# Kernel optimization log

Hardware: AMD Instinct MI355X
Metric: run time of the kernel (lower is better)

## Reference

```python
import jax, jax.numpy as jnp
import numpy as np

N, E, B = 100000, 1600000, 1024
F, H, C = 9, 4, 32
CH, L = 30, 20

def _leaky(x, slope):
    return jnp.where(x >= 0, x, slope * x)

def _add_self_loops(edge_index, n):
    ar = jnp.arange(n, dtype=edge_index.dtype)
    return jnp.concatenate([edge_index, jnp.stack([ar, ar])], axis=1)

def _gat_conv(x, edge_index, W, att_src, att_dst, bias):
    # PyG GATConv, concat heads, eval mode (no attn dropout), self loops
    n = x.shape[0]
    ei = _add_self_loops(edge_index, n)
    src, dst = ei[0], ei[1]
    h = (x @ W).reshape(n, H, C)                      # [N,H,C]
    a_s = jnp.sum(h * att_src, axis=-1)               # [N,H]
    a_d = jnp.sum(h * att_dst, axis=-1)               # [N,H]
    e = _leaky(a_s[src] + a_d[dst], 0.2)              # [Etot,H]
    m = jax.ops.segment_max(e, dst, num_segments=n)
    ex = jnp.exp(e - m[dst])
    s = jax.ops.segment_sum(ex, dst, num_segments=n)
    alpha = ex / (s[dst] + 1e-16)                     # softmax per dst node/head
    msg = h[src] * alpha[:, :, None]                  # [Etot,H,C]
    out = jax.ops.segment_sum(msg, dst, num_segments=n)
    return out.reshape(n, H * C) + bias

def _gcn_conv(x, edge_index, W, bias):
    # PyG GCNConv: self loops + symmetric normalization
    n = x.shape[0]
    ei = _add_self_loops(edge_index, n)
    src, dst = ei[0], ei[1]
    deg = jax.ops.segment_sum(jnp.ones(ei.shape[1], x.dtype), dst, num_segments=n)
    dinv = jnp.where(deg > 0, jax.lax.rsqrt(deg), 0.0)
    norm = dinv[src] * dinv[dst]                      # [Etot]
    h = x @ W
    out = jax.ops.segment_sum(h[src] * norm[:, None], dst, num_segments=n)
    return out + bias

def _global_mean_pool(x, batch, b):
    s = jax.ops.segment_sum(x, batch, num_segments=b)
    cnt = jax.ops.segment_sum(jnp.ones(x.shape[0], x.dtype), batch, num_segments=b)
    return s / jnp.maximum(cnt, 1.0)[:, None]

def _conv1d(x, w, b):
    # x: [B,Cin,L], w: [Cout,Cin,K], VALID conv
    y = jax.lax.conv_general_dilated(x, w, (1,), 'VALID',
                                     dimension_numbers=('NCH', 'OIH', 'NCH'))
    return y + b[None, :, None]

def _bn_eval(x, g, be, m, v):
    return (x - m[None, :, None]) * jax.lax.rsqrt(v[None, :, None] + 1e-5) * g[None, :, None] + be[None, :, None]

def _forward(x, seq_data, W_gat, att_src, att_dst, b_gat, W2, b2, W3, b3,
             conv1_w, conv1_b, conv2_w, conv2_b,
             bn1_g, bn1_b, bn1_m, bn1_v, bn2_g, bn2_b, bn2_m, bn2_v,
             fc1_W, fc1_b, fus_W, fus_b, cls1_W, cls1_b, cls3_W, cls3_b,
             edge_index, batch):
    slope = 0.01  # nn.LeakyReLU default
    # graph branch
    g = _leaky(_gat_conv(x, edge_index, W_gat, att_src, att_dst, b_gat), slope)
    g = _leaky(_gcn_conv(g, edge_index, W2, b2), slope)
    g = _leaky(_gcn_conv(g, edge_index, W3, b3), slope)
    g = _global_mean_pool(g, batch, B)                # [B,128]
    # sequence branch (eval mode: dropout = identity, BN uses running stats)
    s = _conv1d(seq_data, conv1_w, conv1_b)           # [B,64,18]
    s = _leaky(_bn_eval(s, bn1_g, bn1_b, bn1_m, bn1_v), slope)
    s = _conv1d(s, conv2_w, conv2_b)                  # [B,64,16]
    s = _leaky(_bn_eval(s, bn2_g, bn2_b, bn2_m, bn2_v), slope)
    s = s.reshape(s.shape[0], -1) @ fc1_W + fc1_b     # [B,64]
    # fusion + classifier
    comb = jnp.concatenate([g, s], axis=1)            # [B,192]
    comb = _leaky(comb @ fus_W + fus_b, slope)
    comb = _leaky(comb @ cls1_W + cls1_b, slope)
    return comb @ cls3_W + cls3_b                     # [B,1]

def setup_inputs():
    key = jax.random.key(0)
    ks = jax.random.split(key, 20)
    rn = lambda k, s, sc=0.1: jax.random.normal(k, s, dtype=jnp.float32) * sc
    return {
        'x': rn(ks[0], (N, F), 1.0),
        'edge_index': jax.random.randint(ks[1], (2, E), 0, N, dtype=jnp.int32),
        'batch': jnp.sort(jax.random.randint(ks[2], (N,), 0, B, dtype=jnp.int32)),
        'seq_data': rn(ks[3], (B, CH, L), 1.0),
        'W_gat': rn(ks[4], (F, H * C)), 'att_src': rn(ks[5], (H, C)),
        'att_dst': rn(ks[6], (H, C)), 'b_gat': jnp.zeros(H * C, jnp.float32),
        'W2': rn(ks[7], (H * C, 64)), 'b2': jnp.zeros(64, jnp.float32),
        'W3': rn(ks[8], (64, 128)), 'b3': jnp.zeros(128, jnp.float32),
        'conv1_w': rn(ks[9], (64, CH, 3)), 'conv1_b': jnp.zeros(64, jnp.float32),
        'conv2_w': rn(ks[10], (64, 64, 3)), 'conv2_b': jnp.zeros(64, jnp.float32),
        'bn1_g': jnp.ones(64, jnp.float32), 'bn1_b': jnp.zeros(64, jnp.float32),
        'bn1_m': jnp.zeros(64, jnp.float32), 'bn1_v': jnp.ones(64, jnp.float32),
        'bn2_g': jnp.ones(64, jnp.float32), 'bn2_b': jnp.zeros(64, jnp.float32),
        'bn2_m': jnp.zeros(64, jnp.float32), 'bn2_v': jnp.ones(64, jnp.float32),
        'fc1_W': rn(ks[11], (16 * 64, 64)), 'fc1_b': jnp.zeros(64, jnp.float32),
        'fus_W': rn(ks[12], (192, 128)), 'fus_b': jnp.zeros(128, jnp.float32),
        'cls1_W': rn(ks[13], (128, 64)), 'cls1_b': jnp.zeros(64, jnp.float32),
        'cls3_W': rn(ks[14], (64, 1)), 'cls3_b': jnp.zeros(1, jnp.float32),
    }

def reference(x, edge_index, batch, seq_data, W_gat, att_src, att_dst, b_gat,
              W2, b2, W3, b3, conv1_w, conv1_b, conv2_w, conv2_b,
              bn1_g, bn1_b, bn1_m, bn1_v, bn2_g, bn2_b, bn2_m, bn2_v,
              fc1_W, fc1_b, fus_W, fus_b, cls1_W, cls1_b, cls3_W, cls3_b):
    return _forward(x, seq_data, W_gat, att_src, att_dst, b_gat, W2, b2, W3, b3,
                    conv1_w, conv1_b, conv2_w, conv2_b,
                    bn1_g, bn1_b, bn1_m, bn1_v, bn2_g, bn2_b, bn2_m, bn2_v,
                    fc1_W, fc1_b, fus_W, fus_b, cls1_W, cls1_b, cls3_W, cls3_b,
                    edge_index, batch)
```

## Files before the change

### kernel.cpp

```cpp
#include <hip/hip_runtime.h>

#define NND 100000
#define NED 1600000
#define NB  1024
#define FEAT 9
#define HC 128
#define NBUCK ((NND + 511) / 512)
#define BCAP 12288u
#define BINCHUNK 4096
#define BIN_NBLK ((NED + BINCHUNK - 1) / BINCHUNK)

typedef unsigned short u16;

__device__ __forceinline__ void atomAdd(float* p, float v) {
    __hip_atomic_fetch_add(p, v, __ATOMIC_RELAXED, __HIP_MEMORY_SCOPE_AGENT);
}
__device__ __forceinline__ unsigned atomAddU(unsigned* p, unsigned v) {
    return __hip_atomic_fetch_add(p, v, __ATOMIC_RELAXED, __HIP_MEMORY_SCOPE_AGENT);
}
__device__ __forceinline__ float leaky(float v, float s) { return v >= 0.f ? v : s * v; }
__device__ __forceinline__ float bf2f(u16 u) {
    union { unsigned i; float f; } x; x.i = ((unsigned)u) << 16; return x.f;
}
__device__ __forceinline__ u16 f2bf(float f) {
    union { float f; unsigned i; } x; x.f = f;
    return (u16)((x.i + 0x7fffu + ((x.i >> 16) & 1u)) >> 16);
}
__device__ __forceinline__ float bflo(unsigned u) {
    union { unsigned i; float f; } x; x.i = u << 16; return x.f;
}
__device__ __forceinline__ float bfhi(unsigned u) {
    union { unsigned i; float f; } x; x.i = u & 0xffff0000u; return x.f;
}

typedef __attribute__((ext_vector_type(8))) short bfrag;
typedef __attribute__((ext_vector_type(4))) float ffrag;

__global__ void k_matt(const float* __restrict__ Wg, const float* __restrict__ attS,
                       const float* __restrict__ attD, float* __restrict__ M) {
    int t = threadIdx.x;
    if (t >= 72) return;
    int d = t >= 36 ? 1 : 0;
    int q = t - 36 * d;
    int f = q >> 2, h = q & 3;
    const float* av = d ? attD : attS;
    float s = 0.f;
#pragma unroll
    for (int c = 0; c < 32; ++c) s += Wg[f * HC + h * 32 + c] * av[h * 32 + c];
    M[d * 36 + q] = s;
}

__global__ void k_w2t(const float* __restrict__ W2, const float* __restrict__ W3,
                      const float* __restrict__ Wg,
                      u16* __restrict__ w2t, u16* __restrict__ w3t,
                      u16* __restrict__ wgt, unsigned* __restrict__ bktCur) {
    int i = blockIdx.x * 256 + threadIdx.x;
    int n = i >> 7, k = i & 127;
    w2t[i] = f2bf(W2[k * 64 + n]);
    int n3 = i >> 6, k3 = i & 63;
    w3t[i] = f2bf(W3[k3 * 128 + n3]);
    int col = i >> 6, kk = i & 63;
    int f = kk - 9 * (col >> 5);
    wgt[i] = (f >= 0 && f < 9) ? f2bf(Wg[f * 128 + col]) : (u16)0;
    if (i < NBUCK) bktCur[i] = (unsigned)i * BCAP;
}

__global__ void k_att(const float* __restrict__ x, const float* __restrict__ M,
                      u16* __restrict__ rec, float* __restrict__ a_d) {
    __shared__ float Ms[36], Md[36];
    int t = threadIdx.x;
    if (t < 36) Ms[t] = M[t];
    else if (t < 72) Md[t - 36] = M[t];
    __syncthreads();
    int n = blockIdx.x * 256 + t;
    if (n >= NND) return;
    float xv[FEAT];
#pragma unroll
    for (int f = 0; f < FEAT; ++f) xv[f] = x[n * FEAT + f];
    float s0 = 0, s1 = 0, s2 = 0, s3 = 0, d0 = 0, d1 = 0, d2 = 0, d3 = 0;
#pragma unroll
    for (int f = 0; f < FEAT; ++f) {
        float xf = xv[f];
        s0 += xf * Ms[f * 4 + 0]; s1 += xf * Ms[f * 4 + 1];
        s2 += xf * Ms[f * 4 + 2]; s3 += xf * Ms[f * 4 + 3];
        d0 += xf * Md[f * 4 + 0]; d1 += xf * Md[f * 4 + 1];
        d2 += xf * Md[f * 4 + 2]; d3 += xf * Md[f * 4 + 3];
    }
    u16 v[16];
#pragma unroll
    for (int f = 0; f < FEAT; ++f) v[f] = f2bf(xv[f]);
    v[9] = 0; v[10] = 0; v[11] = 0;
    v[12] = f2bf(s0); v[13] = f2bf(s1); v[14] = f2bf(s2); v[15] = f2bf(s3);
    unsigned pk[8];
#pragma unroll
    for (int i = 0; i < 8; ++i) pk[i] = (unsigned)v[2 * i] | ((unsigned)v[2 * i + 1] << 16);
    uint4* rp = (uint4*)(rec + (size_t)n * 16);
    rp[0] = make_uint4(pk[0], pk[1], pk[2], pk[3]);
    rp[1] = make_uint4(pk[4], pk[5], pk[6], pk[7]);
    ((float4*)a_d)[n] = make_float4(d0, d1, d2, d3);
}

__global__ __launch_bounds__(256) void k_bin(const int* __restrict__ ei,
                                             unsigned* __restrict__ bktCursor,
                                             unsigned* __restrict__ staging) {
    __shared__ unsigned hist[NBUCK];
    __shared__ unsigned gbase[NBUCK];
    int t = threadIdx.x;
    if (t < NBUCK) hist[t] = 0;
    __syncthreads();
    int base = blockIdx.x * BINCHUNK;
    int lim = NED - base;
    int srcv[16], dstv[16];
#pragma unroll
    for (int k = 0; k < 16; ++k) {
        int i = t + k * 256;
        if (i < lim) {
            srcv[k] = ei[base + i];
            dstv[k] = ei[NED + base + i];
            atomicAdd(&hist[dstv[k] >> 9], 1u);
        } else dstv[k] = -1;
    }
    __syncthreads();
    if (t < NBUCK) {
        unsigned c = hist[t];
        gbase[t] = c ? atomAddU(&bktCursor[t], c) : 0u;
    }
    __syncthreads();
    if (t < NBUCK) hist[t] = 0;
    __syncthreads();
#pragma unroll
    for (int k = 0; k < 16; ++k) {
        if (dstv[k] >= 0) {
            int bk = dstv[k] >> 9;
            unsigned off = atomicAdd(&hist[bk], 1u);
            staging[gbase[bk] + off] = ((unsigned)(dstv[k] & 511) << 17) | (unsigned)srcv[k];
        }
    }
}

__global__ __launch_bounds__(512) void k_place(const unsigned* __restrict__ bktCur,
                                               const unsigned* __restrict__ staging,
                                               unsigned* __restrict__ csr,
                                               unsigned* __restrict__ rowptr,
                                               u16* __restrict__ degA,
                                               float* __restrict__ dinv) {
    __shared__ unsigned lh[512];
    __shared__ unsigned ls[512];
    int b = blockIdx.x, t = threadIdx.x;
    unsigned lo = (unsigned)b * BCAP;
    unsigned n = bktCur[b] - lo;
    lh[t] = 0;
    __syncthreads();
    for (unsigned i = t; i < n; i += 512) atomicAdd(&lh[staging[lo + i] >> 17], 1u);
    __syncthreads();
    unsigned v = lh[t];
    ls[t] = v;
    __syncthreads();
    for (int off = 1; off < 512; off <<= 1) {
        unsigned u = (t >= off) ? ls[t - off] : 0u;
        __syncthreads();
        ls[t] += u;
        __syncthreads();
    }
    unsigned excl = ls[t] - v;
    int node = b * 512 + t;
    if (node < NND) {
        rowptr[node] = lo + excl;
        degA[node] = (u16)v;
        dinv[node] = rsqrtf((float)v + 1.f);
    }
    __syncthreads();
    lh[t] = excl;
    __syncthreads();
    for (unsigned i = t; i < n; i += 512) {
        unsigned p = staging[lo + i];
        unsigned pos = atomicAdd(&lh[p >> 17], 1u);
        csr[lo + pos] = p & 0x1FFFFu;
    }
}

__global__ __launch_bounds__(256) void k_gat_g(const unsigned* __restrict__ rowptr,
                                               const u16* __restrict__ degA,
                                               const unsigned* __restrict__ csr,
                                               const u16* __restrict__ rec,
                                               const float* __restrict__ a_d,
                                               u16* __restrict__ zb) {
    int n = blockIdx.x * 4 + (threadIdx.x >> 6);
    int l = threadIdx.x & 63;
    int e = l >> 2;
    int h = l & 3;
    unsigned e0 = rowptr[n];
    int m = (int)degA[n] + 1;
    float adh = a_d[n * 4 + h];
    float acc0 = 0, acc1 = 0, acc2 = 0, acc3 = 0, acc4 = 0, acc5 = 0, acc6 = 0, acc7 = 0, acc8 = 0;
    float den = 0.f;
    const uint4* recp = (const uint4*)rec;
    for (int c = 0; c < m; c += 16) {
        int idx = c + e;
        bool act = idx < m;
        int src = n;
        if (act && idx > 0) src = (int)csr[e0 + idx - 1];
        uint4 lo = recp[(size_t)src * 2];
        uint4 hi = recp[(size_t)src * 2 + 1];
        unsigned pair = (h & 2) ? hi.w : hi.z;
        float asf = (h & 1) ? bfhi(pair) : bflo(pair);
        float w = __expf(leaky(asf + adh, 0.2f));
        if (!act) w = 0.f;
        den += w;
        acc0 += w * bflo(lo.x); acc1 += w * bfhi(lo.x);
        acc2 += w * bflo(lo.y); acc3 += w * bfhi(lo.y);
        acc4 += w * bflo(lo.z); acc5 += w * bfhi(lo.z);
        acc6 += w * bflo(lo.w); acc7 += w * bfhi(lo.w);
        acc8 += w * bflo(hi.x);
    }
#pragma unroll
    for (int mask = 4; mask <= 32; mask <<= 1) {
        den  += __shfl_xor(den,  mask, 64);
        acc0 += __shfl_xor(acc0, mask, 64);
        acc1 += __shfl_xor(acc1, mask, 64);
        acc2 += __shfl_xor(acc2, mask, 64);
        acc3 += __shfl_xor(acc3, mask, 64);
        acc4 += __shfl_xor(acc4, mask, 64);
        acc5 += __shfl_xor(acc5, mask, 64);
        acc6 += __shfl_xor(acc6, mask, 64);
        acc7 += __shfl_xor(acc7, mask, 64);
        acc8 += __shfl_xor(acc8, mask, 64);
    }
    if (l < 4) {
        float inv = 1.f / (den + 1e-16f);
        u16* zp = zb + (size_t)n * 36 + h * 9;
        zp[0] = f2bf(acc0 * inv); zp[1] = f2bf(acc1 * inv); zp[2] = f2bf(acc2 * inv);
        zp[3] = f2bf(acc3 * inv); zp[4] = f2bf(acc4 * inv); zp[5] = f2bf(acc5 * inv);
        zp[6] = f2bf(acc6 * inv); zp[7] = f2bf(acc7 * inv); zp[8] = f2bf(acc8 * inv);
    }
}

__global__ __launch_bounds__(256) void k_fused_h2(const u16* __restrict__ zb,
                                                  const u16* __restrict__ wgt,
                                                  const float* __restrict__ bgv,
                                                  const u16* __restrict__ w2t,
                                                  const float* __restrict__ dinv,
                                                  u16* __restrict__ h2) {
    __shared__ u16 zA[64 * 72];
    __shared__ u16 g1L[64 * 136];
    __shared__ float bgs[HC];
    int t = threadIdx.x;
    int n0 = blockIdx.x * 64;
    int nn = NND - n0; if (nn > 64) nn = 64;
    for (int i = t; i < 64 * 36; i += 256) ((unsigned*)zA)[i] = 0u;
    if (t < HC) bgs[t] = bgv[t];
    __syncthreads();
    const unsigned* zbG = (const unsigned*)zb;
    for (int i = t; i < nn * 18; i += 256) {
        int r = i / 18, c = i - r * 18;
        ((unsigned*)zA)[r * 36 + c] = zbG[(size_t)(n0 + r) * 18 + c];
    }
    __syncthreads();
    int l = t & 63, wv = t >> 6;
    int mr = l & 15, quad = l >> 4;
    union U { uint4 u; bfrag v; };
    {
        bfrag a[2];
#pragma unroll
        for (int ks = 0; ks < 2; ++ks) {
            U uu; uu.u = *(const uint4*)(zA + (wv * 16 + mr) * 72 + ks * 32 + quad * 8);
            a[ks] = uu.v;
        }
#pragma unroll
        for (int ct = 0; ct < 8; ++ct) {
            ffrag c = (ffrag){0.f, 0.f, 0.f, 0.f};
#pragma unroll
            for (int ks = 0; ks < 2; ++ks) {
                U ub; ub.u = *(const uint4*)(wgt + (ct * 16 + mr) * 64 + ks * 32 + quad * 8);
                c = __builtin_amdgcn_mfma_f32_16x16x32_bf16(a[ks], ub.v, c, 0, 0, 0);
            }
            int col = ct * 16 + mr;
            float bc = bgs[col];
#pragma unroll
            for (int r = 0; r < 4; ++r) {
                int row = wv * 16 + quad * 4 + r;
                g1L[row * 136 + col] = f2bf(leaky(c[r] + bc, 0.01f));
            }
        }
    }
    __syncthreads();
    {
        bfrag a[4];
#pragma unroll
        for (int ks = 0; ks < 4; ++ks) {
            U uu; uu.u = *(const uint4*)(g1L + (wv * 16 + mr) * 136 + ks * 32 + quad * 8);
            a[ks] = uu.v;
        }
        ffrag acc[4];
#pragma unroll
        for (int ct = 0; ct < 4; ++ct) acc[ct] = (ffrag){0.f, 0.f, 0.f, 0.f};
#pragma unroll
        for (int ct = 0; ct < 4; ++ct) {
#pragma unroll
            for (int ks = 0; ks < 4; ++ks) {
                U ub; ub.u = *(const uint4*)(w2t + (ct * 16 + mr) * 128 + ks * 32 + quad * 8);
                acc[ct] = __builtin_amdgcn_mfma_f32_16x16x32_bf16(a[ks], ub.v, acc[ct], 0, 0, 0);
            }
        }
        int rbase = n0 + wv * 16 + quad * 4;
        if (rbase < NND) {
            float4 d4 = *(const float4*)(dinv + rbase);
            const float dv[4] = {d4.x, d4.y, d4.z, d4.w};
#pragma unroll
            for (int ct = 0; ct < 4; ++ct)
#pragma unroll
                for (int r = 0; r < 4; ++r)
                    h2[(size_t)(rbase + r) * 64 + ct * 16 + mr] = f2bf(dv[r] * acc[ct][r]);
        }
    }
}

template <int OUTMODE>
__global__ void k_gcn_g(const unsigned* __restrict__ rowptr, const u16* __restrict__ degA,
                        const unsigned* __restrict__ csr,
                        const float* __restrict__ dinv, const u16* __restrict__ hin,
                        const float* __restrict__ bias, u16* __restrict__ hout) {
    int n = blockIdx.x * 4 + (threadIdx.x >> 6);
    int l = threadIdx.x & 63;
    int grp = l >> 4;
    int c = l & 15;
    unsigned e0 = rowptr[n];
    unsigned e1 = e0 + degA[n];
    const uint2* hinU = (const uint2*)hin;
    float a0 = 0, a1 = 0, a2 = 0, a3 = 0;
    if (grp == 0) {
        uint2 u = hinU[(size_t)n * 16 + c];
        a0 = bflo(u.x); a1 = bfhi(u.x); a2 = bflo(u.y); a3 = bfhi(u.y);
    }
    unsigned e = e0;
    for (; e + 8 <= e1; e += 8) {
        unsigned s0 = csr[e + grp];
        unsigned s1 = csr[e + 4 + grp];
        uint2 u0 = hinU[(size_t)s0 * 16 + c];
        uint2 u1 = hinU[(size_t)s1 * 16 + c];
        a0 += bflo(u0.x) + bflo(u1.x); a1 += bfhi(u0.x) + bfhi(u1.x);
        a2 += bflo(u0.y) + bflo(u1.y); a3 += bfhi(u0.y) + bfhi(u1.y);
    }
    for (; e + 4 <= e1; e += 4) {
        unsigned s = csr[e + grp];
        uint2 u = hinU[(size_t)s * 16 + c];
        a0 += bflo(u.x); a1 += bfhi(u.x); a2 += bflo(u.y); a3 += bfhi(u.y);
    }
    if (grp < (int)(e1 - e)) {
        unsigned s = csr[e + grp];
        uint2 u = hinU[(size_t)s * 16 + c];
        a0 += bflo(u.x); a1 += bfhi(u.x); a2 += bflo(u.y); a3 += bfhi(u.y);
    }
#pragma unroll
    for (int mask = 16; mask <= 32; mask <<= 1) {
        a0 += __shfl_xor(a0, mask, 64);
        a1 += __shfl_xor(a1, mask, 64);
        a2 += __shfl_xor(a2, mask, 64);
        a3 += __shfl_xor(a3, mask, 64);
    }
    if (grp == 0) {
        float dn = dinv[n];
        float o0 = dn * a0, o1 = dn * a1, o2 = dn * a2, o3 = dn * a3;
        if (OUTMODE == 1) {
            o0 = leaky(o0 + bias[4 * c],     0.01f) * dn;
            o1 = leaky(o1 + bias[4 * c + 1], 0.01f) * dn;
            o2 = leaky(o2 + bias[4 * c + 2], 0.01f) * dn;
            o3 = leaky(o3 + bias[4 * c + 3], 0.01f) * dn;
        }
        uint2 pk;
        pk.x = (unsigned)f2bf(o0) | ((unsigned)f2bf(o1) << 16);
        pk.y = (unsigned)f2bf(o2) | ((unsigned)f2bf(o3) << 16);
        ((uint2*)hout)[(size_t)n * 16 + c] = pk;
    }
}

__global__ __launch_bounds__(256) void k_gcn2_pool(const u16* __restrict__ agg3,
                                                   const u16* __restrict__ w3t,
                                                   const float* __restrict__ b3,
                                                   const int* __restrict__ batch,
                                                   float* __restrict__ pooled,
                                                   float* __restrict__ cnt) {
    __shared__ u16 rows[64 * 72];
    __shared__ int bts[64];
    __shared__ float b3s[128];
    int t = threadIdx.x;
    int n0 = blockIdx.x * 64;
    int nn = NND - n0; if (nn > 64) nn = 64;
    const uint4* src = (const uint4*)(agg3 + (size_t)n0 * 64);
    for (int i = t; i < 512; i += 256) {
        int r = i >> 3, c8 = i & 7;
        uint4 v = (r < nn) ? src[i] : make_uint4(0u, 0u, 0u, 0u);
        *(uint4*)(rows + r * 72 + c8 * 8) = v;
    }
    if (t < 64) bts[t] = (t < nn) ? batch[n0 + t] : -1;
    if (t < 128) b3s[t] = b3[t];
    __syncthreads();
    int l = t & 63, wv = t >> 6;
    int mr = l & 15, quad = l >> 4;
    union U { uint4 u; bfrag v; };
    bfrag a[2];
#pragma unroll
    for (int ks = 0; ks < 2; ++ks) {
        U uu; uu.u = *(const uint4*)(rows + (wv * 16 + mr) * 72 + ks * 32 + quad * 8);
        a[ks] = uu.v;
    }
    ffrag acc[8];
#pragma unroll
    for (int ct = 0; ct < 8; ++ct) acc[ct] = (ffrag){0.f, 0.f, 0.f, 0.f};
#pragma unroll
    for (int ct = 0; ct < 8; ++ct) {
#pragma unroll
        for (int ks = 0; ks < 2; ++ks) {
            U ub; ub.u = *(const uint4*)(w3t + (ct * 16 + mr) * 64 + ks * 32 + quad * 8);
            acc[ct] = __builtin_amdgcn_mfma_f32_16x16x32_bf16(a[ks], ub.v, acc[ct], 0, 0, 0);
        }
    }
    int rl = wv * 16 + quad * 4;
    int ub = bts[wv * 16];
    bool uni = (ub == bts[wv * 16 + 15]);
#pragma unroll
    for (int ct = 0; ct < 8; ++ct) {
        int col = ct * 16 + mr;
        float bc = b3s[col];
        float g0 = leaky(acc[ct][0] + bc, 0.01f);
        float g1 = leaky(acc[ct][1] + bc, 0.01f);
        float g2 = leaky(acc[ct][2] + bc, 0.01f);
        float g3 = leaky(acc[ct][3] + bc, 0.01f);
        if (uni) {
            float s = g0 + g1 + g2 + g3;
            s += __shfl_xor(s, 16, 64);
            s += __shfl_xor(s, 32, 64);
            if (quad == 0 && ub >= 0) atomAdd(&pooled[ub * 128 + col], s);
        } else {
            float gr[4] = {g0, g1, g2, g3};
            int curb = bts[rl];
            float s = 0.f;
#pragma unroll
            for (int r = 0; r < 4; ++r) {
                int b = bts[rl + r];
                if (b != curb) {
                    if (curb >= 0) atomAdd(&pooled[curb * 128 + col], s);
                    s = 0.f; curb = b;
                }
                s += gr[r];
            }
            if (curb >= 0) atomAdd(&pooled[curb * 128 + col], s);
        }
    }
    if (t < nn) {
        int b = bts[t];
        if (t == 0 || bts[t - 1] != b) {
            int len = 1;
            for (int j = t + 1; j < nn && bts[j] == b; ++j) ++len;
            atomAdd(&cnt[b], (float)len);
        }
    }
}

__global__ void k_seq(const float* __restrict__ seq, const float* __restrict__ w1, const float* __restrict__ c1b,
                      const float* __restrict__ w2, const float* __restrict__ c2b,
                      const float* __restrict__ g1n, const float* __restrict__ b1n,
                      const float* __restrict__ m1n, const float* __restrict__ v1n,
                      const float* __restrict__ g2n, const float* __restrict__ b2n,
                      const float* __restrict__ m2n, const float* __restrict__ v2n,
                      const float* __restrict__ fcW, const float* __restrict__ fcb,
                      float* __restrict__ sfc) {
    __shared__ float xs[30 * 20];
    __shared__ float y1[64 * 18];
    __shared__ float y2[64 * 16];
    __shared__ float red[4][64];
    int t = threadIdx.x;
    int b = blockIdx.x;
    for (int idx = t; idx < 600; idx += 256) xs[idx] = seq[b * 600 + idx];
    __syncthreads();
    for (int idx = t; idx < 64 * 18; idx += 256) {
        int o = idx / 18, l = idx - o * 18;
        float acc = c1b[o];
        for (int i = 0; i < 30; ++i)
#pragma unroll
            for (int k = 0; k < 3; ++k)
                acc += xs[i * 20 + l + k] * w1[o * 90 + i * 3 + k];
        float bn = (acc - m1n[o]) * rsqrtf(v1n[o] + 1e-5f) * g1n[o] + b1n[o];
        y1[idx] = leaky(bn, 0.01f);
    }
    __syncthreads();
    for (int idx = t; idx < 64 * 16; idx += 256) {
        int o = idx >> 4, l = idx & 15;
        float acc = c2b[o];
        for (int i = 0; i < 64; ++i)
#pragma unroll
            for (int k = 0; k < 3; ++k)
                acc += y1[i * 18 + l + k] * w2[o * 192 + i * 3 + k];
        float bn = (acc - m2n[o]) * rsqrtf(v2n[o] + 1e-5f) * g2n[o] + b2n[o];
        y2[idx] = leaky(bn, 0.01f);
    }
    __syncthreads();
    {
        int o = t & 63, part = t >> 6;
        float acc = 0.f;
        for (int j = part * 256; j < part * 256 + 256; ++j)
            acc += y2[j] * fcW[j * 64 + o];
        red[part][o] = acc;
    }
    __syncthreads();
    if (t < 64) sfc[b * 64 + t] = red[0][t] + red[1][t] + red[2][t] + red[3][t] + fcb[t];
}

__global__ void k_final(const float* __restrict__ pooled, const float* __restrict__ cnt,
                        const float* __restrict__ sfc,
                        const float* __restrict__ fusW, const float* __restrict__ fusb,
                        const float* __restrict__ c1W, const float* __restrict__ c1b,
                        const float* __restrict__ c3W, const float* __restrict__ c3b,
                        float* __restrict__ out) {
    __shared__ float comb[192];
    __shared__ float t1[128];
    int t = threadIdx.x;
    int b = blockIdx.x;
    float invc = 1.f / fmaxf(cnt[b], 1.f);
    comb[t] = pooled[b * 128 + t] * invc;
    if (t < 64) comb[128 + t] = sfc[b * 64 + t];
    __syncthreads();
    float acc = fusb[t];
    for (int k = 0; k < 192; ++k) acc += comb[k] * fusW[k * 128 + t];
    t1[t] = leaky(acc, 0.01f);
    __syncthreads();
    if (t < 64) {
        float a2 = c1b[t];
        for (int k = 0; k < 128; ++k) a2 += t1[k] * c1W[k * 64 + t];
        a2 = leaky(a2, 0.01f);
        float p = a2 * c3W[t];
#pragma unroll
        for (int off = 32; off; off >>= 1) p += __shfl_xor(p, off, 64);
        if (t == 0) out[b] = p + c3b[0];
    }
}

extern "C" void kernel_launch(void* const* d_in, const int* in_sizes, int n_in,
                              void* d_out, int out_size, void* d_ws, size_t ws_size,
                              hipStream_t stream) {
    const float* x     = (const float*)d_in[0];
    const int*   ei    = (const int*)d_in[1];
    const int*   batch = (const int*)d_in[2];
    const float* seq   = (const float*)d_in[3];
    const float* Wg    = (const float*)d_in[4];
    const float* attS  = (const float*)d_in[5];
    const float* attD  = (const float*)d_in[6];
    const float* bg    = (const float*)d_in[7];
    const float* W2    = (const float*)d_in[8];
    const float* b2    = (const float*)d_in[9];
    const float* W3    = (const float*)d_in[10];
    const float* b3    = (const float*)d_in[11];
    const float* c1w   = (const float*)d_in[12];
    const float* c1bb  = (const float*)d_in[13];
    const float* c2w   = (const float*)d_in[14];
    const float* c2bb  = (const float*)d_in[15];
    const float* bn1g  = (const float*)d_in[16];
    const float* bn1b  = (const float*)d_in[17];
    const float* bn1m  = (const float*)d_in[18];
    const float* bn1v  = (const float*)d_in[19];
    const float* bn2g  = (const float*)d_in[20];
    const float* bn2b  = (const float*)d_in[21];
    const float* bn2m  = (const float*)d_in[22];
    const float* bn2v  = (const float*)d_in[23];
    const float* fcW   = (const float*)d_in[24];
    const float* fcb   = (const float*)d_in[25];
    const float* fusW  = (const float*)d_in[26];
    const float* fusb  = (const float*)d_in[27];
    const float* cls1W = (const float*)d_in[28];
    const float* cls1b = (const float*)d_in[29];
    const float* cls3W = (const float*)d_in[30];
    const float* cls3b = (const float*)d_in[31];

    char* wsb = (char*)d_ws;
    const size_t N = NND;
    float*    M      = (float*)wsb;
    float*    a_d    = M + 80;
    u16*      rec    = (u16*)(a_d + N * 4);
    float*    dinv   = (float*)(rec + N * 16);
    float*    pooled = dinv + N;
    float*    cnt    = pooled + (size_t)NB * 128;
    unsigned* bktCur = (unsigned*)(cnt + NB);
    unsigned* rowptr = bktCur + 256;
    u16*      degA   = (u16*)(rowptr + N);
    u16*      w2t    = degA + N + 8;
    u16*      w3t    = w2t + 8192;
    u16*      wgt    = w3t + 8192;
    unsigned* staging= (unsigned*)(wgt + 8192);
    unsigned* csr    = staging + (size_t)NBUCK * BCAP;
    u16*      zb     = (u16*)(csr + (size_t)NBUCK * BCAP);
    u16*      h2b    = zb + N * 36 + 16;
    u16*      g2b    = h2b + N * 64;
    u16*      agg3b  = g2b + N * 64;
    float*    sfc    = (float*)(agg3b + N * 64);

    size_t zero_bytes = ((size_t)NB * 128 + NB) * 4;
    hipMemsetAsync(pooled, 0, zero_bytes, stream);

    k_matt<<<1, 128, 0, stream>>>(Wg, attS, attD, M);
    k_w2t<<<32, 256, 0, stream>>>(W2, W3, Wg, w2t, w3t, wgt, bktCur);
    k_att<<<(NND + 255) / 256, 256, 0, stream>>>(x, M, rec, a_d);
    k_bin<<<BIN_NBLK, 256, 0, stream>>>(ei, bktCur, staging);
    k_place<<<NBUCK, 512, 0, stream>>>(bktCur, staging, csr, rowptr, degA, dinv);
    k_gat_g<<<NND / 4, 256, 0, stream>>>(rowptr, degA, csr, rec, a_d, zb);
    k_fused_h2<<<(NND + 63) / 64, 256, 0, stream>>>(zb, wgt, bg, w2t, dinv, h2b);
    k_gcn_g<1><<<NND / 4, 256, 0, stream>>>(rowptr, degA, csr, dinv, h2b, b2, g2b);
    k_gcn_g<0><<<NND / 4, 256, 0, stream>>>(rowptr, degA, csr, dinv, g2b, b2, agg3b);
    k_gcn2_pool<<<(NND + 63) / 64, 256, 0, stream>>>(agg3b, w3t, b3, batch, pooled, cnt);
    k_seq<<<NB, 256, 0, stream>>>(seq, c1w, c1bb, c2w, c2bb, bn1g, bn1b, bn1m, bn1v,
                                  bn2g, bn2b, bn2m, bn2v, fcW, fcb, sfc);
    k_final<<<NB, 128, 0, stream>>>(pooled, cnt, sfc, fusW, fusb, cls1W, cls1b,
                                    cls3W, cls3b, (float*)d_out);
}
```

Before: 441.0 us.

## Run sequence conv1d layers as bf16 MFMA im2col GEMMs with folded batchnorm

```diff
diff --git a/kernel.cpp b/kernel.cpp
--- a/kernel.cpp
+++ b/kernel.cpp
@@ -37,8 +37,22 @@
 typedef __attribute__((ext_vector_type(4))) float ffrag;
 
 __global__ void k_matt(const float* __restrict__ Wg, const float* __restrict__ attS,
-                       const float* __restrict__ attD, float* __restrict__ M) {
+                       const float* __restrict__ attD,
+                       const float* __restrict__ c1b, const float* __restrict__ c2b,
+                       const float* __restrict__ g1n, const float* __restrict__ b1n,
+                       const float* __restrict__ m1n, const float* __restrict__ v1n,
+                       const float* __restrict__ g2n, const float* __restrict__ b2n,
+                       const float* __restrict__ m2n, const float* __restrict__ v2n,
+                       float* __restrict__ M, float* __restrict__ scv) {
     int t = threadIdx.x;
+    if (t < 64) {
+        float s1 = g1n[t] * rsqrtf(v1n[t] + 1e-5f);
+        float s2 = g2n[t] * rsqrtf(v2n[t] + 1e-5f);
+        scv[t] = s1;
+        scv[64 + t] = (c1b[t] - m1n[t]) * s1 + b1n[t];
+        scv[128 + t] = s2;
+        scv[192 + t] = (c2b[t] - m2n[t]) * s2 + b2n[t];
+    }
     if (t >= 72) return;
     int d = t >= 36 ? 1 : 0;
     int q = t - 36 * d;
@@ -52,8 +66,10 @@
 
 __global__ void k_w2t(const float* __restrict__ W2, const float* __restrict__ W3,
                       const float* __restrict__ Wg,
+                      const float* __restrict__ c1w, const float* __restrict__ c2w,
                       u16* __restrict__ w2t, u16* __restrict__ w3t,
-                      u16* __restrict__ wgt, unsigned* __restrict__ bktCur) {
+                      u16* __restrict__ wgt, u16* __restrict__ w1p,
+                      u16* __restrict__ w2c, unsigned* __restrict__ bktCur) {
     int i = blockIdx.x * 256 + threadIdx.x;
     int n = i >> 7, k = i & 127;
     w2t[i] = f2bf(W2[k * 64 + n]);
@@ -62,6 +78,11 @@
     int col = i >> 6, kk = i & 63;
     int f = kk - 9 * (col >> 5);
     wgt[i] = (f >= 0 && f < 9) ? f2bf(Wg[f * 128 + col]) : (u16)0;
+    if (i < 6144) {
+        int o = i / 96, kw = i - o * 96;
+        w1p[i] = (kw < 90) ? f2bf(c1w[o * 90 + kw]) : (u16)0;
+    }
+    for (int j = i; j < 12288; j += 8192) w2c[j] = f2bf(c2w[j]);
     if (i < NBUCK) bktCur[i] = (unsigned)i * BCAP;
 }
 
@@ -457,49 +478,79 @@
     }
 }
 
-__global__ void k_seq(const float* __restrict__ seq, const float* __restrict__ w1, const float* __restrict__ c1b,
-                      const float* __restrict__ w2, const float* __restrict__ c2b,
-                      const float* __restrict__ g1n, const float* __restrict__ b1n,
-                      const float* __restrict__ m1n, const float* __restrict__ v1n,
-                      const float* __restrict__ g2n, const float* __restrict__ b2n,
-                      const float* __restrict__ m2n, const float* __restrict__ v2n,
+__global__ __launch_bounds__(256) void k_seq(const float* __restrict__ seq,
+                      const u16* __restrict__ w1p, const u16* __restrict__ w2c,
+                      const float* __restrict__ scv,
                       const float* __restrict__ fcW, const float* __restrict__ fcb,
                       float* __restrict__ sfc) {
-    __shared__ float xs[30 * 20];
-    __shared__ float y1[64 * 18];
-    __shared__ float y2[64 * 16];
+    __shared__ float xs[600];
+    __shared__ u16 A1[32 * 104];
+    __shared__ u16 y1s[64 * 20];
+    __shared__ u16 A2[16 * 200];
+    __shared__ float y2s[64 * 16];
     __shared__ float red[4][64];
     int t = threadIdx.x;
     int b = blockIdx.x;
-    for (int idx = t; idx < 600; idx += 256) xs[idx] = seq[b * 600 + idx];
-    __syncthreads();
-    for (int idx = t; idx < 64 * 18; idx += 256) {
-        int o = idx / 18, l = idx - o * 18;
-        float acc = c1b[o];
-        for (int i = 0; i < 30; ++i)
-#pragma unroll
-            for (int k = 0; k < 3; ++k)
-                acc += xs[i * 20 + l + k] * w1[o * 90 + i * 3 + k];
-        float bn = (acc - m1n[o]) * rsqrtf(v1n[o] + 1e-5f) * g1n[o] + b1n[o];
-        y1[idx] = leaky(bn, 0.01f);
-    }
-    __syncthreads();
-    for (int idx = t; idx < 64 * 16; idx += 256) {
-        int o = idx >> 4, l = idx & 15;
-        float acc = c2b[o];
-        for (int i = 0; i < 64; ++i)
-#pragma unroll
-            for (int k = 0; k < 3; ++k)
-                acc += y1[i * 18 + l + k] * w2[o * 192 + i * 3 + k];
-        float bn = (acc - m2n[o]) * rsqrtf(v2n[o] + 1e-5f) * g2n[o] + b2n[o];
-        y2[idx] = leaky(bn, 0.01f);
+    for (int i = t; i < 600; i += 256) xs[i] = seq[b * 600 + i];
+    for (int i = t; i < 1664; i += 256) ((unsigned*)A1)[i] = 0u;
+    for (int i = t; i < 1600; i += 256) ((unsigned*)A2)[i] = 0u;
+    __syncthreads();
+    for (int i = t; i < 18 * 90; i += 256) {
+        int l = i / 90, k = i - l * 90;
+        int ch = k / 3, kk = k - ch * 3;
+        A1[l * 104 + k] = f2bf(xs[ch * 20 + l + kk]);
+    }
+    __syncthreads();
+    int l = t & 63, wv = t >> 6;
+    int mr = l & 15, quad = l >> 4;
+    union U { uint4 u; bfrag v; };
+    for (int j = wv; j < 8; j += 4) {
+        int rt = j >> 2, ct = j & 3;
+        ffrag c = (ffrag){0.f, 0.f, 0.f, 0.f};
+#pragma unroll
+        for (int ks = 0; ks < 3; ++ks) {
+            U ua; ua.u = *(const uint4*)(A1 + (rt * 16 + mr) * 104 + ks * 32 + quad * 8);
+            U ub; ub.u = *(const uint4*)(w1p + (ct * 16 + mr) * 96 + ks * 32 + quad * 8);
+            c = __builtin_amdgcn_mfma_f32_16x16x32_bf16(ua.v, ub.v, c, 0, 0, 0);
+        }
+        int col = ct * 16 + mr;
+        float s1 = scv[col], o1 = scv[64 + col];
+#pragma unroll
+        for (int r = 0; r < 4; ++r) {
+            int row = rt * 16 + quad * 4 + r;
+            if (row < 18) y1s[col * 20 + row] = f2bf(leaky(c[r] * s1 + o1, 0.01f));
+        }
+    }
+    __syncthreads();
+    for (int i = t; i < 16 * 192; i += 256) {
+        int ll = i / 192, k = i - ll * 192;
+        int ch = k / 3, kk = k - ch * 3;
+        A2[ll * 200 + k] = y1s[ch * 20 + ll + kk];
+    }
+    __syncthreads();
+    {
+        int ct = wv;
+        ffrag c = (ffrag){0.f, 0.f, 0.f, 0.f};
+#pragma unroll
+        for (int ks = 0; ks < 6; ++ks) {
+            U ua; ua.u = *(const uint4*)(A2 + mr * 200 + ks * 32 + quad * 8);
+            U ub; ub.u = *(const uint4*)(w2c + (ct * 16 + mr) * 192 + ks * 32 + quad * 8);
+            c = __builtin_amdgcn_mfma_f32_16x16x32_bf16(ua.v, ub.v, c, 0, 0, 0);
+        }
+        int col = ct * 16 + mr;
+        float s2 = scv[128 + col], o2 = scv[192 + col];
+#pragma unroll
+        for (int r = 0; r < 4; ++r) {
+            int row = quad * 4 + r;
+            y2s[col * 16 + row] = leaky(c[r] * s2 + o2, 0.01f);
+        }
     }
     __syncthreads();
     {
         int o = t & 63, part = t >> 6;
         float acc = 0.f;
         for (int j = part * 256; j < part * 256 + 256; ++j)
-            acc += y2[j] * fcW[j * 64 + o];
+            acc += y2s[j] * fcW[j * 64 + o];
         red[part][o] = acc;
     }
     __syncthreads();
@@ -574,7 +625,8 @@
     char* wsb = (char*)d_ws;
     const size_t N = NND;
     float*    M      = (float*)wsb;
-    float*    a_d    = M + 80;
+    float*    scv    = M + 80;
+    float*    a_d    = scv + 256;
     u16*      rec    = (u16*)(a_d + N * 4);
     float*    dinv   = (float*)(rec + N * 16);
     float*    pooled = dinv + N;
@@ -585,7 +637,9 @@
     u16*      w2t    = degA + N + 8;
     u16*      w3t    = w2t + 8192;
     u16*      wgt    = w3t + 8192;
-    unsigned* staging= (unsigned*)(wgt + 8192);
+    u16*      w1p    = wgt + 8192;
+    u16*      w2c    = w1p + 6144;
+    unsigned* staging= (unsigned*)(w2c + 12288);
     unsigned* csr    = staging + (size_t)NBUCK * BCAP;
     u16*      zb     = (u16*)(csr + (size_t)NBUCK * BCAP);
     u16*      h2b    = zb + N * 36 + 16;
@@ -596,8 +650,9 @@
     size_t zero_bytes = ((size_t)NB * 128 + NB) * 4;
     hipMemsetAsync(pooled, 0, zero_bytes, stream);
 
-    k_matt<<<1, 128, 0, stream>>>(Wg, attS, attD, M);
-    k_w2t<<<32, 256, 0, stream>>>(W2, W3, Wg, w2t, w3t, wgt, bktCur);
+    k_matt<<<1, 128, 0, stream>>>(Wg, attS, attD, c1bb, c2bb, bn1g, bn1b, bn1m, bn1v,
+                                  bn2g, bn2b, bn2m, bn2v, M, scv);
+    k_w2t<<<32, 256, 0, stream>>>(W2, W3, Wg, c1w, c2w, w2t, w3t, wgt, w1p, w2c, bktCur);
     k_att<<<(NND + 255) / 256, 256, 0, stream>>>(x, M, rec, a_d);
     k_bin<<<BIN_NBLK, 256, 0, stream>>>(ei, bktCur, staging);
     k_place<<<NBUCK, 512, 0, stream>>>(bktCur, staging, csr, rowptr, degA, dinv);
@@ -606,8 +661,7 @@
     k_gcn_g<1><<<NND / 4, 256, 0, stream>>>(rowptr, degA, csr, dinv, h2b, b2, g2b);
     k_gcn_g<0><<<NND / 4, 256, 0, stream>>>(rowptr, degA, csr, dinv, g2b, b2, agg3b);
     k_gcn2_pool<<<(NND + 63) / 64, 256, 0, stream>>>(agg3b, w3t, b3, batch, pooled, cnt);
-    k_seq<<<NB, 256, 0, stream>>>(seq, c1w, c1bb, c2w, c2bb, bn1g, bn1b, bn1m, bn1v,
-                                  bn2g, bn2b, bn2m, bn2v, fcW, fcb, sfc);
+    k_seq<<<NB, 256, 0, stream>>>(seq, w1p, w2c, scv, fcW, fcb, sfc);
     k_final<<<NB, 128, 0, stream>>>(pooled, cnt, sfc, fusW, fusb, cls1W, cls1b,
                                     cls3W, cls3b, (float*)d_out);
 }
```

Measured after the change: 409.1 us (median of 2 runs). -7.2%, faster.
